# Kernel tuning notes

Measured on AMD Instinct MI355X. Metric: run time of the kernel, lower is better.

## Reference

```python
import jax, jax.numpy as jnp
import numpy as np

T, N, E = 24, 50000, 800000
IN_F, HID, OUT_F, K = 11, 128, 3, 2


def setup_inputs() -> dict:
    key = jax.random.key(0)
    ks = jax.random.split(key, 8)
    X_seq = jax.random.normal(ks[0], (T, N, IN_F), jnp.float32)
    # monotone time channel (col 6) so dt = X[t+1][:,6] - X[t][:,6] > 0 in the rollout
    times = 0.1 * jnp.arange(T, dtype=jnp.float32)
    X_seq = X_seq.at[:, :, 6].set(jnp.broadcast_to(times[:, None], (T, N)))
    edge_index = jax.random.randint(ks[1], (2, E), 0, N, dtype=jnp.int32)
    s = 0.1
    Wx = s * jax.random.normal(ks[2], (3, K, IN_F, HID), jnp.float32)
    bx = s * jax.random.normal(ks[3], (3, HID), jnp.float32)
    Wh = s * jax.random.normal(ks[4], (3, K, HID, HID), jnp.float32)
    bh = s * jax.random.normal(ks[5], (3, HID), jnp.float32)
    W_head = s * jax.random.normal(ks[6], (HID, OUT_F), jnp.float32)
    b_head = s * jax.random.normal(ks[7], (OUT_F,), jnp.float32)
    return {"X_seq": X_seq, "edge_index": edge_index, "Wx": Wx, "bx": bx,
            "Wh": Wh, "bh": bh, "W_head": W_head, "b_head": b_head}


def reference(X_seq, edge_index, Wx, bx, Wh, bh, W_head, b_head):
    n = X_seq.shape[1]
    src, dst = edge_index[0], edge_index[1]
    # PyG ChebConv sym-normalized scaled Laplacian with lambda_max=2:
    # L_hat = -D^{-1/2} A D^{-1/2}  (zero diagonal)
    deg = jax.ops.segment_sum(jnp.ones(src.shape[0], X_seq.dtype), src, num_segments=n)
    dinv = jnp.where(deg > 0, 1.0 / jnp.sqrt(deg), 0.0)
    w = -(dinv[src] * dinv[dst])  # [E]

    def lap(x):  # x: [N, F] -> L_hat @ x via gather/scatter over edges
        return jax.ops.segment_sum(w[:, None] * x[src], dst, num_segments=n)

    def cheb(x, W, b):  # K=2 ChebConv: Tx0 @ W0 + (L_hat x) @ W1 + bias
        return x @ W[0] + lap(x) @ W[1] + b

    def gru(x, h):  # GConvGRU cell
        z = jax.nn.sigmoid(cheb(x, Wx[0], bx[0]) + cheb(h, Wh[0], bh[0]))
        r = jax.nn.sigmoid(cheb(x, Wx[1], bx[1]) + cheb(h, Wh[1], bh[1]))
        h_tilde = jnp.tanh(cheb(x, Wx[2], bx[2]) + cheb(h * r, Wh[2], bh[2]))
        return z * h + (1.0 - z) * h_tilde

    hid = W_head.shape[0]
    h0 = gru(X_seq[0], jnp.zeros((n, hid), X_seq.dtype))
    u0 = h0 @ W_head + b_head  # [N, 3]
    dt = X_seq[1:, :, 6] - X_seq[:-1, :, 6]  # [T-1, N]

    def step(carry, inp):
        h, u_prev, prev_pos = carry
        x_orig, dt_t = inp
        pos = jax.lax.stop_gradient(u_prev)        # next_u = u.detach()
        vel = (pos - prev_pos) / dt_t[:, None]     # X[t+1][:,8:11]
        x = jnp.concatenate([x_orig[:, :3], pos, x_orig[:, 6:8], vel], axis=1)
        h = gru(x, h)
        u = h @ W_head + b_head
        return (h, u, pos), u

    _, outs = jax.lax.scan(step, (h0, u0, X_seq[0, :, 3:6]), (X_seq[1:], dt))
    return jnp.concatenate([u0[None], outs], axis=0)  # [T, N, 3]
```

## Files before the change

kernel.cpp:

```cpp
#include <hip/hip_runtime.h>
#include <math.h>

#define NN 50000
#define EE 800000
#define TT 24
#define INF 11
#define HID 128

static constexpr int KTOT = 280;
#define BM 64
#define BN 128
#define BK 8
static constexpr int NSTEP = KTOT / BK;

__device__ __forceinline__ float fast_sigmoid(float v) {
    float e = __expf(-v);
    return __builtin_amdgcn_rcpf(1.0f + e);
}
__device__ __forceinline__ float fast_tanh(float v) {
    float e2 = __expf(2.0f * v);
    return 1.0f - 2.0f * __builtin_amdgcn_rcpf(e2 + 1.0f);
}


__global__ void count_deg_kernel(const int* __restrict__ src, const int* __restrict__ dst,
                                 int* __restrict__ deg_src, int* __restrict__ cnt_dst) {
    int e = blockIdx.x * blockDim.x + threadIdx.x;
    if (e < EE) {
        atomicAdd(&deg_src[src[e]], 1);
        atomicAdd(&cnt_dst[dst[e]], 1);
    }
}

__global__ void dinv_kernel(const int* __restrict__ deg, float* __restrict__ dinv) {
    int i = blockIdx.x * blockDim.x + threadIdx.x;
    if (i < NN) {
        int d = deg[i];
        dinv[i] = (d > 0) ? 1.0f / sqrtf((float)d) : 0.0f;
    }
}

__global__ void scan_kernel(const int* __restrict__ cnt, int* __restrict__ row_ptr) {
    __shared__ int buf[2][1024];
    __shared__ int carry_s;
    int tid = threadIdx.x;
    if (tid == 0) carry_s = 0;
    __syncthreads();
    for (int base = 0; base < NN; base += 1024) {
        int i = base + tid;
        int v = (i < NN) ? cnt[i] : 0;
        int pb = 0;
        buf[0][tid] = v;
        __syncthreads();
        for (int off = 1; off < 1024; off <<= 1) {
            int t = buf[pb][tid] + ((tid >= off) ? buf[pb][tid - off] : 0);
            buf[pb ^ 1][tid] = t;
            pb ^= 1;
            __syncthreads();
        }
        int incl = buf[pb][tid];
        int carry = carry_s;
        if (i < NN) row_ptr[i] = carry + incl - v;
        __syncthreads();
        if (tid == 0) carry_s = carry + buf[pb][1023];
        __syncthreads();
    }
    if (tid == 0) row_ptr[NN] = carry_s;
}

__global__ void fill_csr_kernel(const int* __restrict__ src, const int* __restrict__ dst,
                                const int* __restrict__ row_ptr, int* __restrict__ fillp,
                                const float* __restrict__ dinv,
                                int2* __restrict__ csr) {
    int e = blockIdx.x * blockDim.x + threadIdx.x;
    if (e < EE) {
        int s = src[e], d = dst[e];
        int p = row_ptr[d] + atomicAdd(&fillp[d], 1);
        float w = -(dinv[s] * dinv[d]);
        csr[p] = make_int2(s, __float_as_int(w));
    }
}

__global__ void pack_weights_kernel(const float* __restrict__ Wx, const float* __restrict__ bx,
                                    const float* __restrict__ Wh, const float* __restrict__ bh,
                                    float* __restrict__ WA, float* __restrict__ biasA,
                                    float* __restrict__ WB, float* __restrict__ biasB) {
    int idx = blockIdx.x * blockDim.x + threadIdx.x;
    const int NA = 280 * 256, NB = 280 * 128;
    if (idx < NA) {
        int k = idx / 256, j = idx % 256;
        int g = j >> 7, jj = j & 127;
        float v = 0.0f;
        if (k < 12)       { if (k < 11)      v = Wx[((g*2 + 0)*11 + k)      * 128 + jj]; }
        else if (k < 24)  { int kk = k - 12; if (kk < 11) v = Wx[((g*2 + 1)*11 + kk) * 128 + jj]; }
        else if (k < 152) { int kk = k - 24;  v = Wh[((g*2 + 0)*128 + kk) * 128 + jj]; }
        else              { int kk = k - 152; v = Wh[((g*2 + 1)*128 + kk) * 128 + jj]; }
        WA[idx] = v;
    } else if (idx < NA + NB) {
        int t = idx - NA;
        int k = t / 128, jj = t % 128;
        float v = 0.0f;
        if (k < 12)       { if (k < 11)      v = Wx[(4*11 + k)  * 128 + jj]; }
        else if (k < 24)  { int kk = k - 12; if (kk < 11) v = Wx[(5*11 + kk) * 128 + jj]; }
        else if (k < 152) { int kk = k - 24;  v = Wh[(4*128 + kk) * 128 + jj]; }
        else              { int kk = k - 152; v = Wh[(5*128 + kk) * 128 + jj]; }
        WB[t] = v;
    } else if (idx < NA + NB + 256) {
        int j = idx - (NA + NB);
        int g = j >> 7, jj = j & 127;
        biasA[j] = bx[g*128 + jj] + bh[g*128 + jj];
    } else if (idx < NA + NB + 256 + 128) {
        int jj = idx - (NA + NB + 256);
        biasB[jj] = bx[2*128 + jj] + bh[2*128 + jj];
    }
}


__global__ void copy_x0_kernel(const float* __restrict__ X0, float* __restrict__ x) {
    int i = blockIdx.x * blockDim.x + threadIdx.x;
    if (i < NN) {
        #pragma unroll
        for (int c = 0; c < 11; c++) x[i*12 + c] = X0[i*11 + c];
        x[i*12 + 11] = 0.0f;
    }
}

__global__ void build_x_kernel(const float* __restrict__ Xt, const float* __restrict__ Xtm1,
                               const float* __restrict__ pos, const float* __restrict__ prevbase,
                               int prev_stride, int prev_off, float* __restrict__ x) {
    int i = blockIdx.x * blockDim.x + threadIdx.x;
    if (i >= NN) return;
    const float* xo = Xt + (size_t)i * 11;
    float tnow  = xo[6];
    float tprev = Xtm1[(size_t)i * 11 + 6];
    float inv = 1.0f / (tnow - tprev);
    float p0 = pos[(size_t)i*3 + 0], p1 = pos[(size_t)i*3 + 1], p2 = pos[(size_t)i*3 + 2];
    const float* pp = prevbase + (size_t)i * prev_stride + prev_off;
    float q0 = pp[0], q1 = pp[1], q2 = pp[2];
    float* xr = x + (size_t)i * 12;
    xr[0] = xo[0]; xr[1] = xo[1]; xr[2] = xo[2];
    xr[3] = p0;    xr[4] = p1;    xr[5] = p2;
    xr[6] = tnow;  xr[7] = xo[7];
    xr[8] = (p0 - q0) * inv; xr[9] = (p1 - q1) * inv; xr[10] = (p2 - q2) * inv;
    xr[11] = 0.0f;
}

__global__ void lap_small_kernel(const int* __restrict__ row_ptr, const int2* __restrict__ csr,
                                 const float* __restrict__ x, float* __restrict__ xl) {
    int node = blockIdx.x * 16 + (threadIdx.x >> 4);
    int f = threadIdx.x & 15;
    if (node >= NN) return;
    int b = row_ptr[node], e = row_ptr[node + 1];
    float acc = 0.0f;
    for (int p = b; p < e; p++) {
        int2 ed = csr[p];
        float w = __int_as_float(ed.y);
        if (f < 12) acc += w * x[(size_t)ed.x*12 + f];
    }
    if (f < 12) xl[(size_t)node*12 + f] = acc;
}

__global__ __launch_bounds__(256)
void lap_big_kernel(const int* __restrict__ row_ptr, const int2* __restrict__ csr,
                    const float* __restrict__ hin, float* __restrict__ hout) {
    int tid  = threadIdx.x;
    int node = blockIdx.x * 4 + (tid >> 6);
    if (node >= NN) return;
    int eo = (tid >> 5) & 1;
    int f  = tid & 31;
    const float4* h4 = (const float4*)hin;
    float4 acc0 = make_float4(0.f, 0.f, 0.f, 0.f);
    float4 acc1 = make_float4(0.f, 0.f, 0.f, 0.f);
    int b = row_ptr[node], e = row_ptr[node + 1];
    int p = b;
    for (; p + 3 < e; p += 4) {
        int2 ea = csr[p + eo];
        int2 eb = csr[p + 2 + eo];
        float wa = __int_as_float(ea.y);
        float wb = __int_as_float(eb.y);
        float4 va = h4[(size_t)ea.x*32 + f];
        float4 vb = h4[(size_t)eb.x*32 + f];
        acc0.x += wa * va.x; acc0.y += wa * va.y; acc0.z += wa * va.z; acc0.w += wa * va.w;
        acc1.x += wb * vb.x; acc1.y += wb * vb.y; acc1.z += wb * vb.z; acc1.w += wb * vb.w;
    }
    for (; p + 1 < e; p += 2) {
        int2 ea = csr[p + eo];
        float wa = __int_as_float(ea.y);
        float4 va = h4[(size_t)ea.x*32 + f];
        acc0.x += wa * va.x; acc0.y += wa * va.y; acc0.z += wa * va.z; acc0.w += wa * va.w;
    }
    if (p < e && eo == 0) {
        int2 ea = csr[p];
        float wa = __int_as_float(ea.y);
        float4 va = h4[(size_t)ea.x*32 + f];
        acc0.x += wa * va.x; acc0.y += wa * va.y; acc0.z += wa * va.z; acc0.w += wa * va.w;
    }
    acc0.x += acc1.x; acc0.y += acc1.y; acc0.z += acc1.z; acc0.w += acc1.w;
    acc0.x += __shfl_xor(acc0.x, 32);
    acc0.y += __shfl_xor(acc0.y, 32);
    acc0.z += __shfl_xor(acc0.z, 32);
    acc0.w += __shfl_xor(acc0.w, 32);
    if (eo == 0)
        ((float4*)hout)[(size_t)node*32 + f] = acc0;
}

__device__ __forceinline__ float2 loadA2(const float* __restrict__ x, const float* __restrict__ xl,
                                         const float* __restrict__ a2, const float* __restrict__ a3,
                                         int row, int k) {
    if (k < 12)  return *(const float2*)(x  + (size_t)row*12  + k);
    if (k < 24)  return *(const float2*)(xl + (size_t)row*12  + (k - 12));
    if (k < 152) return *(const float2*)(a2 + (size_t)row*128 + (k - 24));
    return *(const float2*)(a3 + (size_t)row*128 + (k - 152));
}

template<int NOUT, int EPI>
__global__ __launch_bounds__(256)
void gemm_kernel(const float* __restrict__ x, const float* __restrict__ xl,
                 const float* __restrict__ a2, const float* __restrict__ a3,
                 const float* __restrict__ W, const float* __restrict__ bias,
                 float* __restrict__ p0, float* __restrict__ p1,
                 const float* __restrict__ p2)
{
    __shared__ float As[2][BK][BM];
    __shared__ float Bs[2][BK][BN];
    const int tid = threadIdx.x;
    const int row0 = blockIdx.x * BM;
    const int col0 = blockIdx.y * BN;
    const int tn_g = tid & 31;
    const int tm_g = tid >> 5;
    const int lm = tid >> 2;
    const int kp = (tid & 3) * 2;
    int arow = row0 + lm; if (arow >= NN) arow = NN - 1;
    const int kb = tid >> 5;
    const int cb = (tid & 31) * 4;

    float acc[8][4];
    #pragma unroll
    for (int i = 0; i < 8; i++) { acc[i][0]=0.f; acc[i][1]=0.f; acc[i][2]=0.f; acc[i][3]=0.f; }

    float2 av = loadA2(x, xl, a2, a3, arow, kp);
    float4 bv = *(const float4*)(W + (size_t)kb * NOUT + col0 + cb);
    As[0][kp][lm]     = av.x;
    As[0][kp + 1][lm] = av.y;
    *(float4*)(&Bs[0][kb][cb]) = bv;
    __syncthreads();

    int bb = 0;
    for (int s = 0; s < NSTEP; s++) {
        float2 av2; float4 bv2;
        if (s + 1 < NSTEP) {
            int kn = (s + 1) * BK;
            av2 = loadA2(x, xl, a2, a3, arow, kn + kp);
            bv2 = *(const float4*)(W + (size_t)(kn + kb) * NOUT + col0 + cb);
        }
        #pragma unroll
        for (int kk = 0; kk < BK; kk++) {
            float4 a0 = *(const float4*)(&As[bb][kk][tm_g*8]);
            float4 a1 = *(const float4*)(&As[bb][kk][tm_g*8 + 4]);
            float4 b  = *(const float4*)(&Bs[bb][kk][tn_g*4]);
            float av_[8] = {a0.x, a0.y, a0.z, a0.w, a1.x, a1.y, a1.z, a1.w};
            float bv_[4] = {b.x, b.y, b.z, b.w};
            #pragma unroll
            for (int i = 0; i < 8; i++)
                #pragma unroll
                for (int j = 0; j < 4; j++)
                    acc[i][j] += av_[i] * bv_[j];
        }
        if (s + 1 < NSTEP) {
            As[bb ^ 1][kp][lm]     = av2.x;
            As[bb ^ 1][kp + 1][lm] = av2.y;
            *(float4*)(&Bs[bb ^ 1][kb][cb]) = bv2;
            __syncthreads();
            bb ^= 1;
        }
    }

    #pragma unroll
    for (int i = 0; i < 8; i++) {
        int row = row0 + tm_g*8 + i;
        if (row >= NN) continue;
        #pragma unroll
        for (int j = 0; j < 4; j++) {
            int col = col0 + tn_g*4 + j;
            float v = acc[i][j] + bias[col];
            if (EPI == 0) {
                float s = fast_sigmoid(v);
                if (col < HID) {
                    p0[(size_t)row*HID + col] = s;
                } else {
                    int c = col - HID;
                    p1[(size_t)row*HID + c] = p2[(size_t)row*HID + c] * s;
                }
            } else {
                float ht = fast_tanh(v);
                float zz   = p0[(size_t)row*HID + col];
                float hold = p1[(size_t)row*HID + col];
                p1[(size_t)row*HID + col] = zz*hold + (1.0f - zz)*ht;
            }
        }
    }
}

__global__ void head_kernel(const float* __restrict__ h, const float* __restrict__ Whead,
                            const float* __restrict__ bhead, float* __restrict__ out) {
    int node = blockIdx.x * 4 + (threadIdx.x >> 6);
    int lane = threadIdx.x & 63;
    if (node >= NN) return;
    float h0 = h[(size_t)node*128 + lane];
    float h1 = h[(size_t)node*128 + 64 + lane];
    float p[3];
    #pragma unroll
    for (int j = 0; j < 3; j++)
        p[j] = h0 * Whead[lane*3 + j] + h1 * Whead[(64 + lane)*3 + j];
    #pragma unroll
    for (int off = 32; off > 0; off >>= 1) {
        p[0] += __shfl_down(p[0], off);
        p[1] += __shfl_down(p[1], off);
        p[2] += __shfl_down(p[2], off);
    }
    if (lane == 0) {
        out[(size_t)node*3 + 0] = p[0] + bhead[0];
        out[(size_t)node*3 + 1] = p[1] + bhead[1];
        out[(size_t)node*3 + 2] = p[2] + bhead[2];
    }
}


extern "C" void kernel_launch(void* const* d_in, const int* in_sizes, int n_in,
                              void* d_out, int out_size, void* d_ws, size_t ws_size,
                              hipStream_t stream) {
    const float* X_seq  = (const float*)d_in[0];
    const int*   eidx   = (const int*)  d_in[1];
    const float* Wx     = (const float*)d_in[2];
    const float* bx     = (const float*)d_in[3];
    const float* Wh     = (const float*)d_in[4];
    const float* bh     = (const float*)d_in[5];
    const float* Whead  = (const float*)d_in[6];
    const float* bhead  = (const float*)d_in[7];
    float* out = (float*)d_out;

    const int* src = eidx;
    const int* dst = eidx + EE;

    char* base = (char*)d_ws;
    size_t off = 0;
    auto carve = [&](size_t bytes) -> void* {
        void* p = base + off;
        off += (bytes + 255) & ~(size_t)255;
        return p;
    };
    int*   deg_i   = (int*)  carve((size_t)NN * 4);
    int*   cnt     = (int*)  carve((size_t)NN * 4);
    int*   fillp   = (int*)  carve((size_t)NN * 4);
    int*   row_ptr = (int*)  carve((size_t)(NN + 1) * 4);
    float* dinv    = (float*)carve((size_t)NN * 4);
    int2*  csr     = (int2*) carve((size_t)EE * 8);
    float* WA      = (float*)carve((size_t)280 * 256 * 4);
    float* biasA   = (float*)carve(256 * 4);
    float* WB      = (float*)carve((size_t)280 * 128 * 4);
    float* biasB   = (float*)carve(128 * 4);
    float* xbuf    = (float*)carve((size_t)NN * 12 * 4);
    float* xlbuf   = (float*)carve((size_t)NN * 12 * 4);
    float* hbuf    = (float*)carve((size_t)NN * 128 * 4);
    float* hlbuf   = (float*)carve((size_t)NN * 128 * 4);
    float* hrbuf   = (float*)carve((size_t)NN * 128 * 4);
    float* zbuf    = (float*)carve((size_t)NN * 128 * 4);
    float* hrlbuf  = hlbuf;
    (void)ws_size; (void)n_in; (void)in_sizes; (void)out_size;

    hipMemsetAsync(deg_i, 0, (size_t)NN * 4, stream);
    hipMemsetAsync(cnt,   0, (size_t)NN * 4, stream);
    hipMemsetAsync(fillp, 0, (size_t)NN * 4, stream);
    hipMemsetAsync(hbuf,  0, (size_t)NN * 128 * 4, stream);

    count_deg_kernel<<<(EE + 255) / 256, 256, 0, stream>>>(src, dst, deg_i, cnt);
    dinv_kernel<<<(NN + 255) / 256, 256, 0, stream>>>(deg_i, dinv);
    scan_kernel<<<1, 1024, 0, stream>>>(cnt, row_ptr);
    fill_csr_kernel<<<(EE + 255) / 256, 256, 0, stream>>>(src, dst, row_ptr, fillp, dinv, csr);
    {
        int total = 280*256 + 280*128 + 256 + 128;
        pack_weights_kernel<<<(total + 255) / 256, 256, 0, stream>>>(Wx, bx, Wh, bh, WA, biasA, WB, biasB);
    }

    const int gridN256 = (NN + 255) / 256;
    const dim3 gridGA((NN + BM - 1) / BM, 2);
    const dim3 gridGB((NN + BM - 1) / BM, 1);

    for (int t = 0; t < TT; t++) {
        if (t == 0) {
            copy_x0_kernel<<<gridN256, 256, 0, stream>>>(X_seq, xbuf);
        } else {
            const float* Xt   = X_seq + (size_t)t * NN * 11;
            const float* Xtm1 = X_seq + (size_t)(t - 1) * NN * 11;
            const float* pos  = out + (size_t)(t - 1) * NN * 3;
            const float* prevbase;
            int pstride, poff;
            if (t == 1) { prevbase = X_seq; pstride = 11; poff = 3; }
            else        { prevbase = out + (size_t)(t - 2) * NN * 3; pstride = 3; poff = 0; }
            build_x_kernel<<<gridN256, 256, 0, stream>>>(Xt, Xtm1, pos, prevbase, pstride, poff, xbuf);
        }

        lap_small_kernel<<<(NN + 15) / 16, 256, 0, stream>>>(row_ptr, csr, xbuf, xlbuf);
        lap_big_kernel<<<(NN + 3) / 4, 256, 0, stream>>>(row_ptr, csr, hbuf, hlbuf);

        gemm_kernel<256, 0><<<gridGA, 256, 0, stream>>>(xbuf, xlbuf, hbuf, hlbuf, WA, biasA,
                                                        zbuf, hrbuf, hbuf);
        lap_big_kernel<<<(NN + 3) / 4, 256, 0, stream>>>(row_ptr, csr, hrbuf, hrlbuf);

        gemm_kernel<128, 1><<<gridGB, 256, 0, stream>>>(xbuf, xlbuf, hrbuf, hrlbuf, WB, biasB,
                                                        zbuf, hbuf, nullptr);

        head_kernel<<<(NN + 3) / 4, 256, 0, stream>>>(hbuf, Whead, bhead, out + (size_t)t * NN * 3);
    }
}
```

Baseline: 8.145 ms.

## Replace FP32 SIMT GEMM with split-bf16 MFMA GEMM and packed operand layout

The FP32 shared-memory GEMM is replaced by an MFMA kernel built on 16x16x32 bf16 instructions. Each fp32 value is split into three bf16 terms and six cross-products are accumulated to approximate fp32 accuracy. Producers (build_x, lap kernels, GEMM epilogues) now write operands directly into padded, K-concatenated bf16 hi/mid/lo arrays, with weights pre-transposed and split. This moves the matrix math onto the matrix cores. In exchange the epilogues and Laplacian kernels write about three times as many bytes, GEMM operands are read straight from global memory without LDS tiling, and results carry a small precision risk.

```diff
diff --git a/kernel.cpp b/kernel.cpp
--- a/kernel.cpp
+++ b/kernel.cpp
@@ -1,17 +1,16 @@
 #include <hip/hip_runtime.h>
+#include <hip/hip_bf16.h>
 #include <math.h>
 
 #define NN 50000
 #define EE 800000
 #define TT 24
-#define INF 11
 #define HID 128
 
-static constexpr int KTOT = 280;
-#define BM 64
-#define BN 128
-#define BK 8
-static constexpr int NSTEP = KTOT / BK;
+static constexpr int KTOT = 288;
+
+typedef __attribute__((ext_vector_type(8))) short v8s;
+typedef __attribute__((ext_vector_type(4))) float v4f;
 
 __device__ __forceinline__ float fast_sigmoid(float v) {
     float e = __expf(-v);
@@ -20,6 +19,20 @@
 __device__ __forceinline__ float fast_tanh(float v) {
     float e2 = __expf(2.0f * v);
     return 1.0f - 2.0f * __builtin_amdgcn_rcpf(e2 + 1.0f);
+}
+
+__device__ __forceinline__ unsigned short f2bf(float v) {
+    __hip_bfloat16 b = __float2bfloat16(v);
+    return *reinterpret_cast<unsigned short*>(&b);
+}
+__device__ __forceinline__ float bf2f(unsigned short u) {
+    __hip_bfloat16 b = *reinterpret_cast<__hip_bfloat16*>(&u);
+    return __bfloat162float(b);
+}
+__device__ __forceinline__ void split3(float v, unsigned short& u0, unsigned short& u1, unsigned short& u2) {
+    u0 = f2bf(v);  float r1 = v - bf2f(u0);
+    u1 = f2bf(r1); float r2 = r1 - bf2f(u1);
+    u2 = f2bf(r2);
 }
 
 
@@ -83,51 +96,69 @@
 
 __global__ void pack_weights_kernel(const float* __restrict__ Wx, const float* __restrict__ bx,
                                     const float* __restrict__ Wh, const float* __restrict__ bh,
-                                    float* __restrict__ WA, float* __restrict__ biasA,
-                                    float* __restrict__ WB, float* __restrict__ biasB) {
+                                    unsigned short* __restrict__ WA0, unsigned short* __restrict__ WA1,
+                                    unsigned short* __restrict__ WA2,
+                                    unsigned short* __restrict__ WB0, unsigned short* __restrict__ WB1,
+                                    unsigned short* __restrict__ WB2,
+                                    float* __restrict__ biasA, float* __restrict__ biasB) {
+    const int NAW = 256 * KTOT, NBW = 128 * KTOT;
     int idx = blockIdx.x * blockDim.x + threadIdx.x;
-    const int NA = 280 * 256, NB = 280 * 128;
-    if (idx < NA) {
-        int k = idx / 256, j = idx % 256;
+    if (idx < NAW) {
+        int j = idx / KTOT, k = idx % KTOT;
         int g = j >> 7, jj = j & 127;
-        float v = 0.0f;
-        if (k < 12)       { if (k < 11)      v = Wx[((g*2 + 0)*11 + k)      * 128 + jj]; }
-        else if (k < 24)  { int kk = k - 12; if (kk < 11) v = Wx[((g*2 + 1)*11 + kk) * 128 + jj]; }
-        else if (k < 152) { int kk = k - 24;  v = Wh[((g*2 + 0)*128 + kk) * 128 + jj]; }
-        else              { int kk = k - 152; v = Wh[((g*2 + 1)*128 + kk) * 128 + jj]; }
-        WA[idx] = v;
-    } else if (idx < NA + NB) {
-        int t = idx - NA;
-        int k = t / 128, jj = t % 128;
-        float v = 0.0f;
-        if (k < 12)       { if (k < 11)      v = Wx[(4*11 + k)  * 128 + jj]; }
-        else if (k < 24)  { int kk = k - 12; if (kk < 11) v = Wx[(5*11 + kk) * 128 + jj]; }
-        else if (k < 152) { int kk = k - 24;  v = Wh[(4*128 + kk) * 128 + jj]; }
-        else              { int kk = k - 152; v = Wh[(5*128 + kk) * 128 + jj]; }
-        WB[t] = v;
-    } else if (idx < NA + NB + 256) {
-        int j = idx - (NA + NB);
+        float v;
+        if (k < 16)       v = (k < 11) ? Wx[((g*2 + 0)*11 + k) * 128 + jj] : 0.0f;
+        else if (k < 32)  { int kk = k - 16; v = (kk < 11) ? Wx[((g*2 + 1)*11 + kk) * 128 + jj] : 0.0f; }
+        else if (k < 160) v = Wh[((g*2 + 0)*128 + (k - 32)) * 128 + jj];
+        else              v = Wh[((g*2 + 1)*128 + (k - 160)) * 128 + jj];
+        unsigned short u0, u1, u2; split3(v, u0, u1, u2);
+        WA0[idx] = u0; WA1[idx] = u1; WA2[idx] = u2;
+    } else if (idx < NAW + NBW) {
+        int t = idx - NAW;
+        int j = t / KTOT, k = t % KTOT;
+        int jj = j;
+        float v;
+        if (k < 16)       v = (k < 11) ? Wx[(4*11 + k) * 128 + jj] : 0.0f;
+        else if (k < 32)  { int kk = k - 16; v = (kk < 11) ? Wx[(5*11 + kk) * 128 + jj] : 0.0f; }
+        else if (k < 160) v = Wh[(4*128 + (k - 32)) * 128 + jj];
+        else              v = Wh[(5*128 + (k - 160)) * 128 + jj];
+        unsigned short u0, u1, u2; split3(v, u0, u1, u2);
+        WB0[t] = u0; WB1[t] = u1; WB2[t] = u2;
+    } else if (idx < NAW + NBW + 256) {
+        int j = idx - (NAW + NBW);
         int g = j >> 7, jj = j & 127;
         biasA[j] = bx[g*128 + jj] + bh[g*128 + jj];
-    } else if (idx < NA + NB + 256 + 128) {
-        int jj = idx - (NA + NB + 256);
+    } else if (idx < NAW + NBW + 256 + 128) {
+        int jj = idx - (NAW + NBW + 256);
         biasB[jj] = bx[2*128 + jj] + bh[2*128 + jj];
     }
 }
 
 
-__global__ void copy_x0_kernel(const float* __restrict__ X0, float* __restrict__ x) {
+__global__ void copy_x0_kernel(const float* __restrict__ Xin, float* __restrict__ xbuf,
+                               unsigned short* __restrict__ X0p, unsigned short* __restrict__ X1p,
+                               unsigned short* __restrict__ X2p) {
     int i = blockIdx.x * blockDim.x + threadIdx.x;
-    if (i < NN) {
-        #pragma unroll
-        for (int c = 0; c < 11; c++) x[i*12 + c] = X0[i*11 + c];
-        x[i*12 + 11] = 0.0f;
+    if (i >= NN) return;
+    float vals[16];
+    #pragma unroll
+    for (int c = 0; c < 11; c++) vals[c] = Xin[(size_t)i*11 + c];
+    #pragma unroll
+    for (int c = 11; c < 16; c++) vals[c] = 0.0f;
+    #pragma unroll
+    for (int c = 0; c < 16; c++) {
+        xbuf[(size_t)i*16 + c] = vals[c];
+        unsigned short u0, u1, u2; split3(vals[c], u0, u1, u2);
+        X0p[(size_t)i*32 + c] = u0; X1p[(size_t)i*32 + c] = u1; X2p[(size_t)i*32 + c] = u2;
     }
 }
 
 __global__ void build_x_kernel(const float* __restrict__ Xt, const float* __restrict__ Xtm1,
                                const float* __restrict__ pos, const float* __restrict__ prevbase,
-                               int prev_stride, int prev_off, float* __restrict__ x) {
+                               int prev_stride, int prev_off,
+                               float* __restrict__ xbuf,
+                               unsigned short* __restrict__ X0p, unsigned short* __restrict__ X1p,
+                               unsigned short* __restrict__ X2p) {
     int i = blockIdx.x * blockDim.x + threadIdx.x;
     if (i >= NN) return;
     const float* xo = Xt + (size_t)i * 11;
@@ -136,17 +167,24 @@
     float inv = 1.0f / (tnow - tprev);
     float p0 = pos[(size_t)i*3 + 0], p1 = pos[(size_t)i*3 + 1], p2 = pos[(size_t)i*3 + 2];
     const float* pp = prevbase + (size_t)i * prev_stride + prev_off;
-    float q0 = pp[0], q1 = pp[1], q2 = pp[2];
-    float* xr = x + (size_t)i * 12;
-    xr[0] = xo[0]; xr[1] = xo[1]; xr[2] = xo[2];
-    xr[3] = p0;    xr[4] = p1;    xr[5] = p2;
-    xr[6] = tnow;  xr[7] = xo[7];
-    xr[8] = (p0 - q0) * inv; xr[9] = (p1 - q1) * inv; xr[10] = (p2 - q2) * inv;
-    xr[11] = 0.0f;
+    float vals[16];
+    vals[0] = xo[0]; vals[1] = xo[1]; vals[2] = xo[2];
+    vals[3] = p0;    vals[4] = p1;    vals[5] = p2;
+    vals[6] = tnow;  vals[7] = xo[7];
+    vals[8] = (p0 - pp[0]) * inv; vals[9] = (p1 - pp[1]) * inv; vals[10] = (p2 - pp[2]) * inv;
+    vals[11] = vals[12] = vals[13] = vals[14] = vals[15] = 0.0f;
+    #pragma unroll
+    for (int c = 0; c < 16; c++) {
+        xbuf[(size_t)i*16 + c] = vals[c];
+        unsigned short u0, u1, u2; split3(vals[c], u0, u1, u2);
+        X0p[(size_t)i*32 + c] = u0; X1p[(size_t)i*32 + c] = u1; X2p[(size_t)i*32 + c] = u2;
+    }
 }
 
 __global__ void lap_small_kernel(const int* __restrict__ row_ptr, const int2* __restrict__ csr,
-                                 const float* __restrict__ x, float* __restrict__ xl) {
+                                 const float* __restrict__ xbuf,
+                                 unsigned short* __restrict__ X0p, unsigned short* __restrict__ X1p,
+                                 unsigned short* __restrict__ X2p) {
     int node = blockIdx.x * 16 + (threadIdx.x >> 4);
     int f = threadIdx.x & 15;
     if (node >= NN) return;
@@ -154,15 +192,19 @@
     float acc = 0.0f;
     for (int p = b; p < e; p++) {
         int2 ed = csr[p];
-        float w = __int_as_float(ed.y);
-        if (f < 12) acc += w * x[(size_t)ed.x*12 + f];
-    }
-    if (f < 12) xl[(size_t)node*12 + f] = acc;
+        acc += __int_as_float(ed.y) * xbuf[(size_t)ed.x*16 + f];
+    }
+    unsigned short u0, u1, u2; split3(acc, u0, u1, u2);
+    X0p[(size_t)node*32 + 16 + f] = u0;
+    X1p[(size_t)node*32 + 16 + f] = u1;
+    X2p[(size_t)node*32 + 16 + f] = u2;
 }
 
 __global__ __launch_bounds__(256)
 void lap_big_kernel(const int* __restrict__ row_ptr, const int2* __restrict__ csr,
-                    const float* __restrict__ hin, float* __restrict__ hout) {
+                    const float* __restrict__ hin,
+                    unsigned short* __restrict__ H0p, unsigned short* __restrict__ H1p,
+                    unsigned short* __restrict__ H2p) {
     int tid  = threadIdx.x;
     int node = blockIdx.x * 4 + (tid >> 6);
     if (node >= NN) return;
@@ -200,105 +242,132 @@
     acc0.y += __shfl_xor(acc0.y, 32);
     acc0.z += __shfl_xor(acc0.z, 32);
     acc0.w += __shfl_xor(acc0.w, 32);
-    if (eo == 0)
-        ((float4*)hout)[(size_t)node*32 + f] = acc0;
-}
-
-__device__ __forceinline__ float2 loadA2(const float* __restrict__ x, const float* __restrict__ xl,
-                                         const float* __restrict__ a2, const float* __restrict__ a3,
-                                         int row, int k) {
-    if (k < 12)  return *(const float2*)(x  + (size_t)row*12  + k);
-    if (k < 24)  return *(const float2*)(xl + (size_t)row*12  + (k - 12));
-    if (k < 152) return *(const float2*)(a2 + (size_t)row*128 + (k - 24));
-    return *(const float2*)(a3 + (size_t)row*128 + (k - 152));
+    if (eo == 0) {
+        size_t base = (size_t)node*256 + 128 + f*4;
+        float a[4] = {acc0.x, acc0.y, acc0.z, acc0.w};
+        ushort4 s0, s1, s2;
+        unsigned short u0, u1, u2;
+        split3(a[0], u0, u1, u2); s0.x = u0; s1.x = u1; s2.x = u2;
+        split3(a[1], u0, u1, u2); s0.y = u0; s1.y = u1; s2.y = u2;
+        split3(a[2], u0, u1, u2); s0.z = u0; s1.z = u1; s2.z = u2;
+        split3(a[3], u0, u1, u2); s0.w = u0; s1.w = u1; s2.w = u2;
+        *(ushort4*)(H0p + base) = s0;
+        *(ushort4*)(H1p + base) = s1;
+        *(ushort4*)(H2p + base) = s2;
+    }
 }
 
 template<int NOUT, int EPI>
 __global__ __launch_bounds__(256)
-void gemm_kernel(const float* __restrict__ x, const float* __restrict__ xl,
-                 const float* __restrict__ a2, const float* __restrict__ a3,
-                 const float* __restrict__ W, const float* __restrict__ bias,
-                 float* __restrict__ p0, float* __restrict__ p1,
-                 const float* __restrict__ p2)
+void gemm_mfma_kernel(const unsigned short* __restrict__ X0p, const unsigned short* __restrict__ X1p,
+                      const unsigned short* __restrict__ X2p,
+                      const unsigned short* __restrict__ H0p, const unsigned short* __restrict__ H1p,
+                      const unsigned short* __restrict__ H2p,
+                      const unsigned short* __restrict__ W0, const unsigned short* __restrict__ W1,
+                      const unsigned short* __restrict__ W2,
+                      const float* __restrict__ bias,
+                      float* __restrict__ p0, float* __restrict__ p1, const float* __restrict__ p2,
+                      unsigned short* __restrict__ S0, unsigned short* __restrict__ S1,
+                      unsigned short* __restrict__ S2)
 {
-    __shared__ float As[2][BK][BM];
-    __shared__ float Bs[2][BK][BN];
-    const int tid = threadIdx.x;
-    const int row0 = blockIdx.x * BM;
-    const int col0 = blockIdx.y * BN;
-    const int tn_g = tid & 31;
-    const int tm_g = tid >> 5;
-    const int lm = tid >> 2;
-    const int kp = (tid & 3) * 2;
-    int arow = row0 + lm; if (arow >= NN) arow = NN - 1;
-    const int kb = tid >> 5;
-    const int cb = (tid & 31) * 4;
-
-    float acc[8][4];
-    #pragma unroll
-    for (int i = 0; i < 8; i++) { acc[i][0]=0.f; acc[i][1]=0.f; acc[i][2]=0.f; acc[i][3]=0.f; }
-
-    float2 av = loadA2(x, xl, a2, a3, arow, kp);
-    float4 bv = *(const float4*)(W + (size_t)kb * NOUT + col0 + cb);
-    As[0][kp][lm]     = av.x;
-    As[0][kp + 1][lm] = av.y;
-    *(float4*)(&Bs[0][kb][cb]) = bv;
-    __syncthreads();
-
-    int bb = 0;
-    for (int s = 0; s < NSTEP; s++) {
-        float2 av2; float4 bv2;
-        if (s + 1 < NSTEP) {
-            int kn = (s + 1) * BK;
-            av2 = loadA2(x, xl, a2, a3, arow, kn + kp);
-            bv2 = *(const float4*)(W + (size_t)(kn + kb) * NOUT + col0 + cb);
-        }
+    const int tid  = threadIdx.x;
+    const int lane = tid & 63, wid = tid >> 6;
+    const int l15 = lane & 15, chunk = lane >> 4;
+    const int row0 = blockIdx.x * 64 + (wid >> 1) * 32;
+    const int col0 = blockIdx.y * 64 + (wid & 1) * 32;
+    int ar0 = row0 + l15;      if (ar0 >= NN) ar0 = NN - 1;
+    int ar1 = row0 + 16 + l15; if (ar1 >= NN) ar1 = NN - 1;
+    const int bc0 = col0 + l15, bc1 = col0 + 16 + l15;
+
+    v4f acc[2][2];
+    v4f z4 = {0.f, 0.f, 0.f, 0.f};
+    acc[0][0] = z4; acc[0][1] = z4; acc[1][0] = z4; acc[1][1] = z4;
+
+    v8s a0[2], a1[2], a2[2], b0[2], b1[2], b2[2];
+
+    {
+        size_t oa0 = (size_t)ar0*32 + chunk*8, oa1 = (size_t)ar1*32 + chunk*8;
+        size_t ob0 = (size_t)bc0*KTOT + chunk*8, ob1 = (size_t)bc1*KTOT + chunk*8;
+        a0[0] = *(const v8s*)(X0p + oa0); a1[0] = *(const v8s*)(X1p + oa0); a2[0] = *(const v8s*)(X2p + oa0);
+        a0[1] = *(const v8s*)(X0p + oa1); a1[1] = *(const v8s*)(X1p + oa1); a2[1] = *(const v8s*)(X2p + oa1);
+        b0[0] = *(const v8s*)(W0 + ob0);  b1[0] = *(const v8s*)(W1 + ob0);  b2[0] = *(const v8s*)(W2 + ob0);
+        b0[1] = *(const v8s*)(W0 + ob1);  b1[1] = *(const v8s*)(W1 + ob1);  b2[1] = *(const v8s*)(W2 + ob1);
         #pragma unroll
-        for (int kk = 0; kk < BK; kk++) {
-            float4 a0 = *(const float4*)(&As[bb][kk][tm_g*8]);
-            float4 a1 = *(const float4*)(&As[bb][kk][tm_g*8 + 4]);
-            float4 b  = *(const float4*)(&Bs[bb][kk][tn_g*4]);
-            float av_[8] = {a0.x, a0.y, a0.z, a0.w, a1.x, a1.y, a1.z, a1.w};
-            float bv_[4] = {b.x, b.y, b.z, b.w};
+        for (int mi = 0; mi < 2; mi++)
             #pragma unroll
-            for (int i = 0; i < 8; i++)
-                #pragma unroll
-                for (int j = 0; j < 4; j++)
-                    acc[i][j] += av_[i] * bv_[j];
-        }
-        if (s + 1 < NSTEP) {
-            As[bb ^ 1][kp][lm]     = av2.x;
-            As[bb ^ 1][kp + 1][lm] = av2.y;
-            *(float4*)(&Bs[bb ^ 1][kb][cb]) = bv2;
-            __syncthreads();
-            bb ^= 1;
-        }
-    }
-
-    #pragma unroll
-    for (int i = 0; i < 8; i++) {
-        int row = row0 + tm_g*8 + i;
-        if (row >= NN) continue;
+            for (int ni = 0; ni < 2; ni++) {
+                v4f c = acc[mi][ni];
+                c = __builtin_amdgcn_mfma_f32_16x16x32_bf16(a0[mi], b0[ni], c, 0, 0, 0);
+                c = __builtin_amdgcn_mfma_f32_16x16x32_bf16(a0[mi], b1[ni], c, 0, 0, 0);
+                c = __builtin_amdgcn_mfma_f32_16x16x32_bf16(a1[mi], b0[ni], c, 0, 0, 0);
+                c = __builtin_amdgcn_mfma_f32_16x16x32_bf16(a0[mi], b2[ni], c, 0, 0, 0);
+                c = __builtin_amdgcn_mfma_f32_16x16x32_bf16(a1[mi], b1[ni], c, 0, 0, 0);
+                c = __builtin_amdgcn_mfma_f32_16x16x32_bf16(a2[mi], b0[ni], c, 0, 0, 0);
+                acc[mi][ni] = c;
+            }
+    }
+    #pragma unroll
+    for (int ks = 1; ks < 9; ks++) {
+        int ka = (ks - 1) * 32 + chunk * 8;
+        int kb = ks * 32 + chunk * 8;
+        size_t oa0 = (size_t)ar0*256 + ka, oa1 = (size_t)ar1*256 + ka;
+        size_t ob0 = (size_t)bc0*KTOT + kb, ob1 = (size_t)bc1*KTOT + kb;
+        a0[0] = *(const v8s*)(H0p + oa0); a1[0] = *(const v8s*)(H1p + oa0); a2[0] = *(const v8s*)(H2p + oa0);
+        a0[1] = *(const v8s*)(H0p + oa1); a1[1] = *(const v8s*)(H1p + oa1); a2[1] = *(const v8s*)(H2p + oa1);
+        b0[0] = *(const v8s*)(W0 + ob0);  b1[0] = *(const v8s*)(W1 + ob0);  b2[0] = *(const v8s*)(W2 + ob0);
+        b0[1] = *(const v8s*)(W0 + ob1);  b1[1] = *(const v8s*)(W1 + ob1);  b2[1] = *(const v8s*)(W2 + ob1);
         #pragma unroll
-        for (int j = 0; j < 4; j++) {
-            int col = col0 + tn_g*4 + j;
-            float v = acc[i][j] + bias[col];
-            if (EPI == 0) {
-                float s = fast_sigmoid(v);
-                if (col < HID) {
-                    p0[(size_t)row*HID + col] = s;
+        for (int mi = 0; mi < 2; mi++)
+            #pragma unroll
+            for (int ni = 0; ni < 2; ni++) {
+                v4f c = acc[mi][ni];
+                c = __builtin_amdgcn_mfma_f32_16x16x32_bf16(a0[mi], b0[ni], c, 0, 0, 0);
+                c = __builtin_amdgcn_mfma_f32_16x16x32_bf16(a0[mi], b1[ni], c, 0, 0, 0);
+                c = __builtin_amdgcn_mfma_f32_16x16x32_bf16(a1[mi], b0[ni], c, 0, 0, 0);
+                c = __builtin_amdgcn_mfma_f32_16x16x32_bf16(a0[mi], b2[ni], c, 0, 0, 0);
+                c = __builtin_amdgcn_mfma_f32_16x16x32_bf16(a1[mi], b1[ni], c, 0, 0, 0);
+                c = __builtin_amdgcn_mfma_f32_16x16x32_bf16(a2[mi], b0[ni], c, 0, 0, 0);
+                acc[mi][ni] = c;
+            }
+    }
+
+    #pragma unroll
+    for (int mi = 0; mi < 2; mi++)
+        #pragma unroll
+        for (int ni = 0; ni < 2; ni++) {
+            int cc = col0 + ni*16 + l15;
+            float bv = bias[cc];
+            #pragma unroll
+            for (int r = 0; r < 4; r++) {
+                int row = row0 + mi*16 + chunk*4 + r;
+                if (row >= NN) continue;
+                float v = acc[mi][ni][r] + bv;
+                if (EPI == 0) {
+                    float s = fast_sigmoid(v);
+                    if (cc < HID) {
+                        p0[(size_t)row*HID + cc] = s;
+                    } else {
+                        int c = cc - HID;
+                        float hr = p2[(size_t)row*HID + c] * s;
+                        p1[(size_t)row*HID + c] = hr;
+                        unsigned short u0, u1, u2; split3(hr, u0, u1, u2);
+                        S0[(size_t)row*256 + c] = u0;
+                        S1[(size_t)row*256 + c] = u1;
+                        S2[(size_t)row*256 + c] = u2;
+                    }
                 } else {
-                    int c = col - HID;
-                    p1[(size_t)row*HID + c] = p2[(size_t)row*HID + c] * s;
+                    float ht = fast_tanh(v);
+                    float zz   = p0[(size_t)row*HID + cc];
+                    float hold = p1[(size_t)row*HID + cc];
+                    float hn = zz*hold + (1.0f - zz)*ht;
+                    p1[(size_t)row*HID + cc] = hn;
+                    unsigned short u0, u1, u2; split3(hn, u0, u1, u2);
+                    S0[(size_t)row*256 + cc] = u0;
+                    S1[(size_t)row*256 + cc] = u1;
+                    S2[(size_t)row*256 + cc] = u2;
                 }
-            } else {
-                float ht = fast_tanh(v);
-                float zz   = p0[(size_t)row*HID + col];
-                float hold = p1[(size_t)row*HID + col];
-                p1[(size_t)row*HID + col] = zz*hold + (1.0f - zz)*ht;
             }
         }
-    }
 }
 
 __global__ void head_kernel(const float* __restrict__ h, const float* __restrict__ Whead,
@@ -355,40 +424,55 @@
     int*   row_ptr = (int*)  carve((size_t)(NN + 1) * 4);
     float* dinv    = (float*)carve((size_t)NN * 4);
     int2*  csr     = (int2*) carve((size_t)EE * 8);
-    float* WA      = (float*)carve((size_t)280 * 256 * 4);
+    unsigned short* WA0 = (unsigned short*)carve((size_t)256 * KTOT * 2);
+    unsigned short* WA1 = (unsigned short*)carve((size_t)256 * KTOT * 2);
+    unsigned short* WA2 = (unsigned short*)carve((size_t)256 * KTOT * 2);
+    unsigned short* WB0 = (unsigned short*)carve((size_t)128 * KTOT * 2);
+    unsigned short* WB1 = (unsigned short*)carve((size_t)128 * KTOT * 2);
+    unsigned short* WB2 = (unsigned short*)carve((size_t)128 * KTOT * 2);
     float* biasA   = (float*)carve(256 * 4);
-    float* WB      = (float*)carve((size_t)280 * 128 * 4);
     float* biasB   = (float*)carve(128 * 4);
-    float* xbuf    = (float*)carve((size_t)NN * 12 * 4);
-    float* xlbuf   = (float*)carve((size_t)NN * 12 * 4);
+    float* xbuf    = (float*)carve((size_t)NN * 16 * 4);
+    unsigned short* X0p = (unsigned short*)carve((size_t)NN * 32 * 2);
+    unsigned short* X1p = (unsigned short*)carve((size_t)NN * 32 * 2);
+    unsigned short* X2p = (unsigned short*)carve((size_t)NN * 32 * 2);
     float* hbuf    = (float*)carve((size_t)NN * 128 * 4);
-    float* hlbuf   = (float*)carve((size_t)NN * 128 * 4);
+    unsigned short* HA0 = (unsigned short*)carve((size_t)NN * 256 * 2);
+    unsigned short* HA1 = (unsigned short*)carve((size_t)NN * 256 * 2);
+    unsigned short* HA2 = (unsigned short*)carve((size_t)NN * 256 * 2);
     float* hrbuf   = (float*)carve((size_t)NN * 128 * 4);
+    unsigned short* HB0 = (unsigned short*)carve((size_t)NN * 256 * 2);
+    unsigned short* HB1 = (unsigned short*)carve((size_t)NN * 256 * 2);
+    unsigned short* HB2 = (unsigned short*)carve((size_t)NN * 256 * 2);
     float* zbuf    = (float*)carve((size_t)NN * 128 * 4);
-    float* hrlbuf  = hlbuf;
     (void)ws_size; (void)n_in; (void)in_sizes; (void)out_size;
 
     hipMemsetAsync(deg_i, 0, (size_t)NN * 4, stream);
     hipMemsetAsync(cnt,   0, (size_t)NN * 4, stream);
     hipMemsetAsync(fillp, 0, (size_t)NN * 4, stream);
     hipMemsetAsync(hbuf,  0, (size_t)NN * 128 * 4, stream);
+    hipMemsetAsync(HA0,   0, (size_t)NN * 256 * 2, stream);
+    hipMemsetAsync(HA1,   0, (size_t)NN * 256 * 2, stream);
+    hipMemsetAsync(HA2,   0, (size_t)NN * 256 * 2, stream);
 
     count_deg_kernel<<<(EE + 255) / 256, 256, 0, stream>>>(src, dst, deg_i, cnt);
     dinv_kernel<<<(NN + 255) / 256, 256, 0, stream>>>(deg_i, dinv);
     scan_kernel<<<1, 1024, 0, stream>>>(cnt, row_ptr);
     fill_csr_kernel<<<(EE + 255) / 256, 256, 0, stream>>>(src, dst, row_ptr, fillp, dinv, csr);
     {
-        int total = 280*256 + 280*128 + 256 + 128;
-        pack_weights_kernel<<<(total + 255) / 256, 256, 0, stream>>>(Wx, bx, Wh, bh, WA, biasA, WB, biasB);
+        int total = 256*KTOT + 128*KTOT + 256 + 128;
+        pack_weights_kernel<<<(total + 255) / 256, 256, 0, stream>>>(Wx, bx, Wh, bh,
+            WA0, WA1, WA2, WB0, WB1, WB2, biasA, biasB);
     }
 
     const int gridN256 = (NN + 255) / 256;
-    const dim3 gridGA((NN + BM - 1) / BM, 2);
-    const dim3 gridGB((NN + BM - 1) / BM, 1);
+    const int gridM = (NN + 63) / 64;
+    const dim3 gridGA(gridM, 4);
+    const dim3 gridGB(gridM, 2);
 
     for (int t = 0; t < TT; t++) {
         if (t == 0) {
-            copy_x0_kernel<<<gridN256, 256, 0, stream>>>(X_seq, xbuf);
+            copy_x0_kernel<<<gridN256, 256, 0, stream>>>(X_seq, xbuf, X0p, X1p, X2p);
         } else {
             const float* Xt   = X_seq + (size_t)t * NN * 11;
             const float* Xtm1 = X_seq + (size_t)(t - 1) * NN * 11;
@@ -397,18 +481,21 @@
             int pstride, poff;
             if (t == 1) { prevbase = X_seq; pstride = 11; poff = 3; }
             else        { prevbase = out + (size_t)(t - 2) * NN * 3; pstride = 3; poff = 0; }
-            build_x_kernel<<<gridN256, 256, 0, stream>>>(Xt, Xtm1, pos, prevbase, pstride, poff, xbuf);
+            build_x_kernel<<<gridN256, 256, 0, stream>>>(Xt, Xtm1, pos, prevbase, pstride, poff,
+                                                         xbuf, X0p, X1p, X2p);
         }
 
-        lap_small_kernel<<<(NN + 15) / 16, 256, 0, stream>>>(row_ptr, csr, xbuf, xlbuf);
-        lap_big_kernel<<<(NN + 3) / 4, 256, 0, stream>>>(row_ptr, csr, hbuf, hlbuf);
-
-        gemm_kernel<256, 0><<<gridGA, 256, 0, stream>>>(xbuf, xlbuf, hbuf, hlbuf, WA, biasA,
-                                                        zbuf, hrbuf, hbuf);
-        lap_big_kernel<<<(NN + 3) / 4, 256, 0, stream>>>(row_ptr, csr, hrbuf, hrlbuf);
-
-        gemm_kernel<128, 1><<<gridGB, 256, 0, stream>>>(xbuf, xlbuf, hrbuf, hrlbuf, WB, biasB,
-                                                        zbuf, hbuf, nullptr);
+        lap_small_kernel<<<(NN + 15) / 16, 256, 0, stream>>>(row_ptr, csr, xbuf, X0p, X1p, X2p);
+        lap_big_kernel<<<(NN + 3) / 4, 256, 0, stream>>>(row_ptr, csr, hbuf, HA0, HA1, HA2);
+
+        gemm_mfma_kernel<256, 0><<<gridGA, 256, 0, stream>>>(X0p, X1p, X2p, HA0, HA1, HA2,
+                                                             WA0, WA1, WA2, biasA,
+                                                             zbuf, hrbuf, hbuf, HB0, HB1, HB2);
+        lap_big_kernel<<<(NN + 3) / 4, 256, 0, stream>>>(row_ptr, csr, hrbuf, HB0, HB1, HB2);
+
+        gemm_mfma_kernel<128, 1><<<gridGB, 256, 0, stream>>>(X0p, X1p, X2p, HB0, HB1, HB2,
+                                                             WB0, WB1, WB2, biasB,
+                                                             zbuf, hbuf, nullptr, HA0, HA1, HA2);
 
         head_kernel<<<(NN + 3) / 4, 256, 0, stream>>>(hbuf, Whead, bhead, out + (size_t)t * NN * 3);
     }
```

Measured after the change: 9.185 ms. 12.8% more time.
